# Kernel optimization log

Hardware: AMD Instinct MI355X
Metric: run time of the kernel (lower is better)

## Reference

```python
import jax, jax.numpy as jnp
import numpy as np

B, S, D = 4, 2048, 1024

def setup_inputs() -> dict:
    key = jax.random.key(0)
    ks = jax.random.split(key, 7)
    s = 1.0 / np.sqrt(D)
    return {
        "x": jax.random.normal(ks[0], (B, S, D), dtype=jnp.float32),
        "Wk": jax.random.uniform(ks[1], (D, D), jnp.float32, -s, s),
        "bk": jax.random.uniform(ks[2], (D,), jnp.float32, -s, s),
        "Wq": jax.random.uniform(ks[3], (D, D), jnp.float32, -s, s),
        "bq": jax.random.uniform(ks[4], (D,), jnp.float32, -s, s),
        "Wv": jax.random.uniform(ks[5], (D, D), jnp.float32, -s, s),
        "bv": jax.random.uniform(ks[6], (D,), jnp.float32, -s, s),
    }

def reference(x, Wk, bk, Wq, bq, Wv, bv):
    # Linear projections (torch Linear: x @ W.T + b; here weights stored as [in, out])
    k = jnp.einsum('bsd,de->bse', x, Wk) + bk
    q = jnp.einsum('bsd,de->bse', x, Wq) + bq
    v = jnp.einsum('bsd,de->bse', x, Wv) + bv
    scale = jnp.asarray(q.shape[-1], q.dtype) ** 0.5
    scores = jnp.einsum('bqd,bkd->bqk', q, k) / scale  # [B,S,S]
    attn = jax.nn.softmax(scores, axis=-1)
    y = jnp.einsum('bqk,bkd->bqd', attn, v)
    return y
```

## Files before the change

kernel.cpp:

```cpp
#include <hip/hip_runtime.h>
#include <hip/hip_bf16.h>


typedef __attribute__((ext_vector_type(8))) short short8;
typedef __attribute__((ext_vector_type(4))) float f32x4;

__device__ __forceinline__ unsigned short f2b(float f) {
    unsigned u = __builtin_bit_cast(unsigned, f);
    unsigned r = 0x7FFFu + ((u >> 16) & 1u);
    return (unsigned short)((u + r) >> 16);
}
__device__ __forceinline__ float b2f(unsigned short h) {
    return __builtin_bit_cast(float, ((unsigned)h) << 16);
}

__device__ __forceinline__ void gload16(const void* g, void* lds_uniform_base) {
    __builtin_amdgcn_global_load_lds(
        (const __attribute__((address_space(1))) unsigned int*)(unsigned long long)g,
        (__attribute__((address_space(3))) unsigned int*)(unsigned)(unsigned long long)lds_uniform_base,
        16, 0, 0);
}

__global__ void cvt_x(const float* __restrict__ x, unsigned short* __restrict__ xb) {
    int i = blockIdx.x * 256 + threadIdx.x;
    float4 v = ((const float4*)x)[i];
    ushort4 o;
    o.x = f2b(v.x); o.y = f2b(v.y); o.z = f2b(v.z); o.w = f2b(v.w);
    ((ushort4*)xb)[i] = o;
}

__global__ void transpose_w(const float* __restrict__ w0, const float* __restrict__ w1,
                            const float* __restrict__ w2, unsigned short* __restrict__ wt) {
    const float* W = (blockIdx.z == 0) ? w0 : (blockIdx.z == 1) ? w1 : w2;
    __shared__ float t[32][33];
    int k0 = blockIdx.y * 32, n0 = blockIdx.x * 32;
    int tx = threadIdx.x, ty = threadIdx.y;
#pragma unroll
    for (int i = 0; i < 4; i++)
        t[ty * 4 + i][tx] = W[(size_t)(k0 + ty * 4 + i) * 1024 + n0 + tx];
    __syncthreads();
    unsigned short* out = wt + (size_t)blockIdx.z * 1024 * 1024;
#pragma unroll
    for (int i = 0; i < 4; i++)
        out[(size_t)(n0 + ty * 4 + i) * 1024 + k0 + tx] = f2b(t[tx][ty * 4 + i]);
}

template <int MODE>
__global__ __launch_bounds__(256, 2) void gemm_nt(
    const unsigned short* __restrict__ A, const unsigned short* __restrict__ Bm,
    void* __restrict__ Cv, const float* __restrict__ bias,
    int N, int K, long long sA, long long sB, long long sC, float alpha) {
    __shared__ unsigned short As[128 * 32];
    __shared__ unsigned short Bs[128 * 32];
    const int tid = threadIdx.x;
    const int wave = tid >> 6, lane = tid & 63;
    const int m0 = blockIdx.y * 128, n0 = blockIdx.x * 128;
    const long long z = blockIdx.z;
    A += z * sA;
    Bm += z * sB;
    const int wm = wave >> 1, wn = wave & 1;
    f32x4 acc[4][4];
#pragma unroll
    for (int i = 0; i < 4; i++)
#pragma unroll
        for (int j = 0; j < 4; j++) acc[i][j] = (f32x4){0.f, 0.f, 0.f, 0.f};

    const int l16 = lane & 15;
    const int lk = (lane >> 4) << 3;

    for (int k0 = 0; k0 < K; k0 += 32) {
#pragma unroll
        for (int j = 0; j < 2; j++) {
            int cid = tid + j * 256;
            int row = cid >> 2, kk = (cid & 3) << 3;
            gload16(A + (size_t)(m0 + row) * K + k0 + kk,
                    (char*)As + wave * 1024 + j * 4096);
            gload16(Bm + (size_t)(n0 + row) * K + k0 + kk,
                    (char*)Bs + wave * 1024 + j * 4096);
        }
        __syncthreads();
        short8 af[4], bf[4];
#pragma unroll
        for (int m = 0; m < 4; m++)
            af[m] = *(const short8*)&As[(wm * 64 + m * 16 + l16) * 32 + lk];
#pragma unroll
        for (int n = 0; n < 4; n++)
            bf[n] = *(const short8*)&Bs[(wn * 64 + n * 16 + l16) * 32 + lk];
#pragma unroll
        for (int m = 0; m < 4; m++)
#pragma unroll
            for (int n = 0; n < 4; n++)
                acc[m][n] = __builtin_amdgcn_mfma_f32_16x16x32_bf16(af[m], bf[n], acc[m][n], 0, 0, 0);
        __syncthreads();
    }

    const int rowb0 = m0 + wm * 64 + ((lane >> 4) << 2);
    const int colb0 = n0 + wn * 64 + l16;
#pragma unroll
    for (int m = 0; m < 4; m++) {
#pragma unroll
        for (int n = 0; n < 4; n++) {
            int col = colb0 + n * 16;
            int rowb = rowb0 + m * 16;
            float bv_ = bias ? bias[col] : 0.f;
            if (MODE == 0) {
                unsigned short* C = (unsigned short*)Cv + z * sC;
#pragma unroll
                for (int i = 0; i < 4; i++)
                    C[(size_t)(rowb + i) * N + col] = f2b(acc[m][n][i] * alpha + bv_);
            } else if (MODE == 2) {
                float* C = (float*)Cv + z * sC;
#pragma unroll
                for (int i = 0; i < 4; i++)
                    C[(size_t)(rowb + i) * N + col] = acc[m][n][i] * alpha + bv_;
            } else {
                int b = rowb >> 11, s = rowb & 2047;
                ushort4 pk;
                pk.x = f2b(acc[m][n][0] * alpha + bv_);
                pk.y = f2b(acc[m][n][1] * alpha + bv_);
                pk.z = f2b(acc[m][n][2] * alpha + bv_);
                pk.w = f2b(acc[m][n][3] * alpha + bv_);
                *(ushort4*)((unsigned short*)Cv + (size_t)b * (1024 * 2048) + (size_t)col * 2048 + s) = pk;
            }
        }
    }
}

__global__ __launch_bounds__(256) void softmax_inplace(unsigned short* __restrict__ sc) {
    const size_t row = blockIdx.x;
    unsigned short* p = sc + row * 2048;
    const int tid = threadIdx.x;
    const int wave = tid >> 6, lane = tid & 63;
    short8 raw = *(const short8*)&p[tid * 8];
    float f[8];
#pragma unroll
    for (int i = 0; i < 8; i++) f[i] = b2f((unsigned short)raw[i]);
    float mx = f[0];
#pragma unroll
    for (int i = 1; i < 8; i++) mx = fmaxf(mx, f[i]);
#pragma unroll
    for (int o = 32; o > 0; o >>= 1) mx = fmaxf(mx, __shfl_xor(mx, o, 64));
    __shared__ float red[8];
    if (lane == 0) red[wave] = mx;
    __syncthreads();
    mx = fmaxf(fmaxf(red[0], red[1]), fmaxf(red[2], red[3]));
    float e[8], s = 0.f;
#pragma unroll
    for (int i = 0; i < 8; i++) { e[i] = __expf(f[i] - mx); s += e[i]; }
#pragma unroll
    for (int o = 32; o > 0; o >>= 1) s += __shfl_xor(s, o, 64);
    if (lane == 0) red[4 + wave] = s;
    __syncthreads();
    s = (red[4] + red[5]) + (red[6] + red[7]);
    float r = 1.0f / s;
    short8 outv;
#pragma unroll
    for (int i = 0; i < 8; i++) outv[i] = (short)f2b(e[i] * r);
    *(short8*)&p[tid * 8] = outv;
}

extern "C" void kernel_launch(void* const* d_in, const int* in_sizes, int n_in,
                              void* d_out, int out_size, void* d_ws, size_t ws_size,
                              hipStream_t stream) {
    const float* x  = (const float*)d_in[0];
    const float* Wk = (const float*)d_in[1];
    const float* bk = (const float*)d_in[2];
    const float* Wq = (const float*)d_in[3];
    const float* bq = (const float*)d_in[4];
    const float* Wv = (const float*)d_in[5];
    const float* bv = (const float*)d_in[6];
    float* out = (float*)d_out;

    char* ws = (char*)d_ws;
    unsigned short* xb  = (unsigned short*)(ws);
    unsigned short* wt  = (unsigned short*)(ws + 16777216);
    unsigned short* kb  = (unsigned short*)(ws + 23068672);
    unsigned short* qb  = (unsigned short*)(ws + 39845888);
    unsigned short* vtb = (unsigned short*)(ws + 56623104);
    unsigned short* sc  = (unsigned short*)(ws + 73400320);

    cvt_x<<<8192, 256, 0, stream>>>(x, xb);
    transpose_w<<<dim3(32, 32, 3), dim3(32, 8), 0, stream>>>(Wk, Wq, Wv, wt);

    gemm_nt<0><<<dim3(8, 64, 1), 256, 0, stream>>>(xb, wt + 0 * 1048576, kb, bk,
                                                   1024, 1024, 0, 0, 0, 1.f);
    gemm_nt<0><<<dim3(8, 64, 1), 256, 0, stream>>>(xb, wt + 1 * 1048576, qb, bq,
                                                   1024, 1024, 0, 0, 0, 1.f);
    gemm_nt<1><<<dim3(8, 64, 1), 256, 0, stream>>>(xb, wt + 2 * 1048576, vtb, bv,
                                                   1024, 1024, 0, 0, 0, 1.f);

    gemm_nt<0><<<dim3(16, 16, 4), 256, 0, stream>>>(qb, kb, sc, nullptr,
                                                    2048, 1024,
                                                    2048LL * 1024, 2048LL * 1024, 2048LL * 2048,
                                                    0.03125f);
    softmax_inplace<<<8192, 256, 0, stream>>>(sc);

    gemm_nt<2><<<dim3(8, 16, 4), 256, 0, stream>>>(sc, vtb, out, nullptr,
                                                   1024, 2048,
                                                   2048LL * 2048, 1024LL * 2048, 2048LL * 1024,
                                                   1.f);
}
```

Before: 303.5 us.

## Use 256-row double-buffered GEMM tiles with XCD-aware block remapping

```diff
diff --git a/kernel.cpp b/kernel.cpp
--- a/kernel.cpp
+++ b/kernel.cpp
@@ -45,71 +45,100 @@
         out[(size_t)(n0 + ty * 4 + i) * 1024 + k0 + tx] = f2b(t[tx][ty * 4 + i]);
 }
 
-template <int MODE>
-__global__ __launch_bounds__(256, 2) void gemm_nt(
+template <int BN, int MODE>
+__global__ __launch_bounds__(512, 2) void gemm2(
     const unsigned short* __restrict__ A, const unsigned short* __restrict__ Bm,
     void* __restrict__ Cv, const float* __restrict__ bias,
     int N, int K, long long sA, long long sB, long long sC, float alpha) {
-    __shared__ unsigned short As[128 * 32];
-    __shared__ unsigned short Bs[128 * 32];
+    constexpr int FN = BN / 64;
+    __shared__ unsigned short As[2][256 * 64];
+    __shared__ unsigned short Bs[2][BN * 64];
     const int tid = threadIdx.x;
     const int wave = tid >> 6, lane = tid & 63;
-    const int m0 = blockIdx.y * 128, n0 = blockIdx.x * 128;
-    const long long z = blockIdx.z;
-    A += z * sA;
-    Bm += z * sB;
-    const int wm = wave >> 1, wn = wave & 1;
-    f32x4 acc[4][4];
-#pragma unroll
-    for (int i = 0; i < 4; i++)
-#pragma unroll
-        for (int j = 0; j < 4; j++) acc[i][j] = (f32x4){0.f, 0.f, 0.f, 0.f};
-
+
+    const int gx = gridDim.x, gy = gridDim.y;
+    const int nwg = gx * gy * (int)gridDim.z;
+    const int orig = blockIdx.x + gx * (blockIdx.y + gy * blockIdx.z);
+    const int q8 = nwg >> 3, r8 = nwg & 7;
+    const int xcd = orig & 7, sub = orig >> 3;
+    const int wg = (xcd < r8 ? xcd * (q8 + 1) : r8 * (q8 + 1) + (xcd - r8) * q8) + sub;
+    const int bx = wg % gx;
+    const int tmp = wg / gx;
+    const int by = tmp % gy, bz = tmp / gy;
+
+    const int m0 = by * 256, n0 = bx * BN;
+    A += (long long)bz * sA;
+    Bm += (long long)bz * sB;
+
+    const int wm = wave >> 2, wn = wave & 3;
     const int l16 = lane & 15;
     const int lk = (lane >> 4) << 3;
 
-    for (int k0 = 0; k0 < K; k0 += 32) {
-#pragma unroll
-        for (int j = 0; j < 2; j++) {
-            int cid = tid + j * 256;
-            int row = cid >> 2, kk = (cid & 3) << 3;
+    f32x4 acc[8][FN];
+#pragma unroll
+    for (int m = 0; m < 8; m++)
+#pragma unroll
+        for (int n = 0; n < FN; n++) acc[m][n] = (f32x4){0.f, 0.f, 0.f, 0.f};
+
+    auto STAGE = [&](int buf, int t) {
+        const int k0 = t << 6;
+#pragma unroll
+        for (int j = 0; j < 4; j++) {
+            int cid = tid + j * 512;
+            int row = cid >> 3, kk = (cid & 7) << 3;
             gload16(A + (size_t)(m0 + row) * K + k0 + kk,
-                    (char*)As + wave * 1024 + j * 4096);
+                    (char*)&As[buf][0] + wave * 1024 + j * 8192);
+        }
+#pragma unroll
+        for (int j = 0; j < FN; j++) {
+            int cid = tid + j * 512;
+            int row = cid >> 3, kk = (cid & 7) << 3;
             gload16(Bm + (size_t)(n0 + row) * K + k0 + kk,
-                    (char*)Bs + wave * 1024 + j * 4096);
+                    (char*)&Bs[buf][0] + wave * 1024 + j * 8192);
+        }
+    };
+
+    const int nt = K >> 6;
+    int cur = 0;
+    STAGE(0, 0);
+    __syncthreads();
+    for (int t = 0; t < nt; ++t) {
+        if (t + 1 < nt) STAGE(cur ^ 1, t + 1);
+#pragma unroll
+        for (int ks = 0; ks < 2; ks++) {
+            short8 af[8], bf[FN];
+#pragma unroll
+            for (int m = 0; m < 8; m++)
+                af[m] = *(const short8*)&As[cur][(wm * 128 + m * 16 + l16) * 64 + ks * 32 + lk];
+#pragma unroll
+            for (int n = 0; n < FN; n++)
+                bf[n] = *(const short8*)&Bs[cur][(wn * (BN / 4) + n * 16 + l16) * 64 + ks * 32 + lk];
+#pragma unroll
+            for (int m = 0; m < 8; m++)
+#pragma unroll
+                for (int n = 0; n < FN; n++)
+                    acc[m][n] = __builtin_amdgcn_mfma_f32_16x16x32_bf16(af[m], bf[n], acc[m][n], 0, 0, 0);
         }
         __syncthreads();
-        short8 af[4], bf[4];
-#pragma unroll
-        for (int m = 0; m < 4; m++)
-            af[m] = *(const short8*)&As[(wm * 64 + m * 16 + l16) * 32 + lk];
-#pragma unroll
-        for (int n = 0; n < 4; n++)
-            bf[n] = *(const short8*)&Bs[(wn * 64 + n * 16 + l16) * 32 + lk];
-#pragma unroll
-        for (int m = 0; m < 4; m++)
-#pragma unroll
-            for (int n = 0; n < 4; n++)
-                acc[m][n] = __builtin_amdgcn_mfma_f32_16x16x32_bf16(af[m], bf[n], acc[m][n], 0, 0, 0);
-        __syncthreads();
+        cur ^= 1;
     }
 
-    const int rowb0 = m0 + wm * 64 + ((lane >> 4) << 2);
-    const int colb0 = n0 + wn * 64 + l16;
-#pragma unroll
-    for (int m = 0; m < 4; m++) {
-#pragma unroll
-        for (int n = 0; n < 4; n++) {
+    const int rowb0 = m0 + wm * 128 + ((lane >> 4) << 2);
+    const int colb0 = n0 + wn * (BN / 4) + l16;
+#pragma unroll
+    for (int m = 0; m < 8; m++) {
+#pragma unroll
+        for (int n = 0; n < FN; n++) {
             int col = colb0 + n * 16;
             int rowb = rowb0 + m * 16;
             float bv_ = bias ? bias[col] : 0.f;
             if (MODE == 0) {
-                unsigned short* C = (unsigned short*)Cv + z * sC;
+                unsigned short* C = (unsigned short*)Cv + (long long)bz * sC;
 #pragma unroll
                 for (int i = 0; i < 4; i++)
                     C[(size_t)(rowb + i) * N + col] = f2b(acc[m][n][i] * alpha + bv_);
             } else if (MODE == 2) {
-                float* C = (float*)Cv + z * sC;
+                float* C = (float*)Cv + (long long)bz * sC;
 #pragma unroll
                 for (int i = 0; i < 4; i++)
                     C[(size_t)(rowb + i) * N + col] = acc[m][n][i] * alpha + bv_;
@@ -182,21 +211,21 @@
     cvt_x<<<8192, 256, 0, stream>>>(x, xb);
     transpose_w<<<dim3(32, 32, 3), dim3(32, 8), 0, stream>>>(Wk, Wq, Wv, wt);
 
-    gemm_nt<0><<<dim3(8, 64, 1), 256, 0, stream>>>(xb, wt + 0 * 1048576, kb, bk,
-                                                   1024, 1024, 0, 0, 0, 1.f);
-    gemm_nt<0><<<dim3(8, 64, 1), 256, 0, stream>>>(xb, wt + 1 * 1048576, qb, bq,
-                                                   1024, 1024, 0, 0, 0, 1.f);
-    gemm_nt<1><<<dim3(8, 64, 1), 256, 0, stream>>>(xb, wt + 2 * 1048576, vtb, bv,
-                                                   1024, 1024, 0, 0, 0, 1.f);
-
-    gemm_nt<0><<<dim3(16, 16, 4), 256, 0, stream>>>(qb, kb, sc, nullptr,
-                                                    2048, 1024,
-                                                    2048LL * 1024, 2048LL * 1024, 2048LL * 2048,
-                                                    0.03125f);
+    gemm2<128, 0><<<dim3(8, 32, 1), 512, 0, stream>>>(xb, wt + 0 * 1048576, kb, bk,
+                                                      1024, 1024, 0, 0, 0, 1.f);
+    gemm2<128, 0><<<dim3(8, 32, 1), 512, 0, stream>>>(xb, wt + 1 * 1048576, qb, bq,
+                                                      1024, 1024, 0, 0, 0, 1.f);
+    gemm2<128, 1><<<dim3(8, 32, 1), 512, 0, stream>>>(xb, wt + 2 * 1048576, vtb, bv,
+                                                      1024, 1024, 0, 0, 0, 1.f);
+
+    gemm2<256, 0><<<dim3(8, 8, 4), 512, 0, stream>>>(qb, kb, sc, nullptr,
+                                                     2048, 1024,
+                                                     2048LL * 1024, 2048LL * 1024, 2048LL * 2048,
+                                                     0.03125f);
     softmax_inplace<<<8192, 256, 0, stream>>>(sc);
 
-    gemm_nt<2><<<dim3(8, 16, 4), 256, 0, stream>>>(sc, vtb, out, nullptr,
-                                                   1024, 2048,
-                                                   2048LL * 2048, 1024LL * 2048, 2048LL * 1024,
-                                                   1.f);
-}
+    gemm2<128, 2><<<dim3(8, 8, 4), 512, 0, stream>>>(sc, vtb, out, nullptr,
+                                                     1024, 2048,
+                                                     2048LL * 2048, 1024LL * 2048, 2048LL * 1024,
+                                                     1.f);
+}
```

Result: faster. 294.6 us (-2.9%).
